# Performance work log

Hardware: AMD Instinct MI355X
Metric: run time of the kernel (lower is better)

## Reference

```python
import jax, jax.numpy as jnp
import numpy as np

RF = 512      # receptive field (power of 2)
F = 128       # filter_size
UP = 200      # upsample_size
MGC = 60      # mgc_size
NB = 4        # num_blocks
NL = 9        # log2(RF) CondConv layers per WaveNet block
T = 4         # number of mgc frames
N = T * UP    # number of sliding windows (800)
SQ = 0.70710678118


def setup_inputs() -> dict:
    key = jax.random.key(0)
    ks = jax.random.split(key, 12)
    r = lambda k, shp, s: jax.random.normal(k, shp, jnp.float32) * s
    return {
        "mgc": r(ks[0], (T, MGC), 1.0),
        "signal": r(ks[1], (N + RF,), 0.5),
        "cond_w": r(ks[2], (MGC * UP, MGC), 0.1),
        "cond_b": jnp.zeros((MGC * UP,), jnp.float32),
        "conv0_w": r(ks[3], (NB, 3, F, 1, 2), 0.3),
        "conv0_b": jnp.zeros((NB, 3, F), jnp.float32),
        "convL_w": r(ks[4], (NB, NL - 1, 3, F, F, 2), 0.08),
        "convL_b": jnp.zeros((NB, NL - 1, 3, F), jnp.float32),
        "condlin_w": r(ks[5], (NB, NL, 2, F, MGC), 0.1),
        "condlin_b": jnp.zeros((NB, NL, 2, F), jnp.float32),
        "pre_w": r(ks[6], (NB, 256, F), 0.08),
        "pre_b": jnp.zeros((NB, 256), jnp.float32),
        "mean_w": r(ks[7], (NB, 1, 256), 0.05),
        "mean_b": jnp.zeros((NB, 1), jnp.float32),
        "std_w": r(ks[8], (NB, 1, 256), 0.05),
        "std_b": jnp.zeros((NB, 1), jnp.float32),
        "eps": r(ks[9], (NB, N, 1), 1.0),
    }


def _cond_conv(h, W, b, cw, cb, cond):
    # h: [N, Cin, L]; W: [3, F, Cin, 2] (input/gate/residual stacked); b: [3, F]
    # kernel=2, stride=2 -> non-overlapping pairs; express as einsum GEMM
    n, c, L = h.shape
    hr = h.reshape(n, c, L // 2, 2)
    o = jnp.einsum('nclk,tock->tnol', hr, W) + b[:, None, :, None]  # [3, N, F, L/2]
    ci = cond @ cw[0].T + cb[0]  # [N, F]
    cg = cond @ cw[1].T + cb[1]  # [N, F]
    it = jnp.tanh(o[0] + ci[:, :, None])
    gt = jax.nn.sigmoid(o[1] + cg[:, :, None])
    return (it * gt + o[2]) * SQ


def _forward(mgc, signal, cond_w, cond_b, conv0_w, conv0_b, convL_w, convL_b,
             condlin_w, condlin_b, pre_w, pre_b, mean_w, mean_b, std_w, std_b, eps):
    # conditioning: Linear(60 -> 60*200) + tanh, reshaped to [T*200, 60]
    cond = jnp.tanh(mgc @ cond_w.T + cond_b).reshape(N, MGC)
    idx = jnp.arange(N)[:, None] + jnp.arange(RF)[None, :]  # sliding windows
    prev = signal
    tails = []
    mean = logvar = None
    for blk in range(NB):
        h = prev[idx][:, None, :]  # [N, 1, RF]
        for l in range(NL):
            W = conv0_w[blk] if l == 0 else convL_w[blk, l - 1]
            bb = conv0_b[blk] if l == 0 else convL_b[blk, l - 1]
            h = _cond_conv(h, W, bb, condlin_w[blk, l], condlin_b[blk, l], cond)
        pre = jax.nn.relu(h[:, :, 0] @ pre_w[blk].T + pre_b[blk])  # [N, 256]
        mean = pre @ mean_w[blk].T + mean_b[blk]    # [N, 1]
        logvar = pre @ std_w[blk].T + std_b[blk]    # [N, 1]
        new_x = eps[blk] * jnp.exp(0.5 * logvar) + mean  # reparameterize
        tails.append(jax.lax.stop_gradient(new_x[-RF:]))  # detached tail
        prev = jnp.concatenate([signal[:RF], new_x[:, 0]])
    return signal[RF:], mean, logvar, jnp.stack(tails)


def reference(mgc, signal, cond_w, cond_b, conv0_w, conv0_b, convL_w, convL_b,
              condlin_w, condlin_b, pre_w, pre_b, mean_w, mean_b, std_w, std_b, eps):
    return _forward(mgc, signal, cond_w, cond_b, conv0_w, conv0_b, convL_w, convL_b,
                    condlin_w, condlin_b, pre_w, pre_b, mean_w, mean_b, std_w, std_b, eps)
```

## Files before the change

kernel.cpp:

```cpp
#include <hip/hip_runtime.h>
#include <hip/hip_bf16.h>

#define F 128
#define MGCS 60
#define NWIN 800
#define RFS 512
#define NBLK 4
#define NLAY 9
#define SQF 0.70710678118f

typedef __attribute__((ext_vector_type(8))) short s16x8;
typedef __attribute__((ext_vector_type(4))) float f32x4;

#define VMCNT(n) asm volatile("s_waitcnt vmcnt(" #n ")" ::: "memory")

__device__ __forceinline__ float gated_act(float o0, float o1, float o2) {
  o0 = fminf(fmaxf(o0, -21.f), 21.f);
  o1 = fminf(fmaxf(o1, -21.f), 21.f);
  float a = __expf(2.f * o0);
  float b = __expf(-o1);
  float r = (a - 1.f) * __builtin_amdgcn_rcpf((a + 1.f) * (1.f + b));
  return (r + o2) * SQF;
}


__global__ void k_cond(const float* __restrict__ mgc, const float* __restrict__ cond_w,
                       const float* __restrict__ cond_b, float* __restrict__ cond) {
  int i = blockIdx.x * blockDim.x + threadIdx.x;
  if (i >= NWIN * MGCS) return;
  int n = i / MGCS, m = i % MGCS;
  int t = n / 200, u = n % 200;
  const float* wrow = cond_w + (size_t)(u * MGCS + m) * MGCS;
  const float* mr = mgc + t * MGCS;
  float s = cond_b[u * MGCS + m];
#pragma unroll
  for (int k = 0; k < MGCS; ++k) s += mr[k] * wrow[k];
  cond[i] = tanhf(s);
}

__global__ __launch_bounds__(256) void k_ci(
    const float* __restrict__ cond, const float* __restrict__ clw,
    const float* __restrict__ clb, float* __restrict__ CI) {
  int w = blockIdx.x;
  int n0 = blockIdx.y * 128;
  __shared__ float wsh[128][61];
  __shared__ float csh[128][61];
  int tid = threadIdx.x;
  for (int idx = tid; idx < 128 * MGCS; idx += 256) {
    int f = idx / MGCS, k = idx % MGCS;
    wsh[f][k] = clw[((size_t)w * 128 + f) * MGCS + k];
  }
  for (int idx = tid; idx < 128 * MGCS; idx += 256) {
    int n = idx / MGCS, k = idx % MGCS;
    csh[n][k] = (n0 + n < NWIN) ? cond[(n0 + n) * MGCS + k] : 0.f;
  }
  __syncthreads();
  int tn = tid >> 4, tf = tid & 15;
  float acc[8][8] = {};
  for (int k = 0; k < MGCS; ++k) {
    float a[8], b[8];
#pragma unroll
    for (int i = 0; i < 8; ++i) a[i] = csh[i * 16 + tn][k];
#pragma unroll
    for (int j = 0; j < 8; ++j) b[j] = wsh[j * 16 + tf][k];
#pragma unroll
    for (int i = 0; i < 8; ++i)
#pragma unroll
      for (int j = 0; j < 8; ++j) acc[i][j] += a[i] * b[j];
  }
  float bb[8];
#pragma unroll
  for (int j = 0; j < 8; ++j) bb[j] = clb[w * 128 + j * 16 + tf];
#pragma unroll
  for (int i = 0; i < 8; ++i) {
    int n = n0 + i * 16 + tn;
    if (n < NWIN) {
#pragma unroll
      for (int j = 0; j < 8; ++j)
        CI[((size_t)w * NWIN + n) * 128 + j * 16 + tf] = acc[i][j] + bb[j];
    }
  }
}

__global__ void k_wt(const float* __restrict__ convL_w, __hip_bfloat16* __restrict__ W2) {
  int i = blockIdx.x * blockDim.x + threadIdx.x;
  const int total = NBLK * 8 * 384 * 256;
  if (i >= total) return;
  int k = i & 255;
  int tf = (i >> 8) % 384;
  int wl = i / (384 * 256);
  int t = tf >> 7, f = tf & 127;
  int k2 = k >> 7, c = k & 127;
  W2[i] = __float2bfloat16(convL_w[(((size_t)(wl * 3 + t) * 128 + f) * 128 + c) * 2 + k2]);
}

__global__ void k_wt2(const float* __restrict__ pre_w, __hip_bfloat16* __restrict__ PW) {
  int i = blockIdx.x * blockDim.x + threadIdx.x;
  if (i < NBLK * 256 * 128) PW[i] = __float2bfloat16(pre_w[i]);
}

__global__ void k_outsig(const float* __restrict__ signal, float* __restrict__ out) {
  int i = blockIdx.x * blockDim.x + threadIdx.x;
  if (i < NWIN) out[i] = signal[RFS + i];
}


__global__ void k_pre0(const float* __restrict__ prev, const float* __restrict__ w0,
                       const float* __restrict__ b0, float* __restrict__ CV) {
  int i = blockIdx.x * blockDim.x + threadIdx.x;
  if (i >= 1310 * 384) return;
  int tf = i % 384, s = i / 384;
  CV[i] = b0[tf] + prev[s] * w0[tf * 2] + prev[s + 1] * w0[tf * 2 + 1];
}

__global__ void k_layer0(const float* __restrict__ CV, const float* __restrict__ CIb,
                         __hip_bfloat16* __restrict__ out) {
  int i = blockIdx.x * blockDim.x + threadIdx.x;
  if (i >= NWIN * 256 * 16) return;
  int fg = i & 15;
  int rest = i >> 4;
  int j = rest & 255;
  int n = rest >> 8;
  int f0 = fg * 8;
  const float* cv = CV + (size_t)(n + 2 * j) * 384;
  const float* ci = CIb + (size_t)n * F;
  float4 c0a = *(const float4*)(cv + f0),       c0b = *(const float4*)(cv + f0 + 4);
  float4 c1a = *(const float4*)(cv + 128 + f0), c1b = *(const float4*)(cv + 132 + f0);
  float4 c2a = *(const float4*)(cv + 256 + f0), c2b = *(const float4*)(cv + 260 + f0);
  float4 i0a = *(const float4*)(ci + f0),       i0b = *(const float4*)(ci + f0 + 4);
  float4 i1a = *(const float4*)(ci + (size_t)NWIN * F + f0);
  float4 i1b = *(const float4*)(ci + (size_t)NWIN * F + f0 + 4);
  s16x8 res;
#pragma unroll
  for (int e = 0; e < 8; ++e) {
    float o0 = ((e < 4) ? (&c0a.x)[e] : (&c0b.x)[e - 4]) + ((e < 4) ? (&i0a.x)[e] : (&i0b.x)[e - 4]);
    float o1 = ((e < 4) ? (&c1a.x)[e] : (&c1b.x)[e - 4]) + ((e < 4) ? (&i1a.x)[e] : (&i1b.x)[e - 4]);
    float o2 = (e < 4) ? (&c2a.x)[e] : (&c2b.x)[e - 4];
    __hip_bfloat16 h = __float2bfloat16(gated_act(o0, o1, o2));
    res[e] = *(short*)&h;
  }
  *(s16x8*)(out + ((size_t)(n * 256 + j)) * F + f0) = res;
}

template <int MFR, bool FLAT>
__device__ __forceinline__ void fuse_layer_b(
    const char* src, char* dst, const s16x8 (&breg)[3][8],
    const float* __restrict__ bb, const float* __restrict__ ciA,
    const float* __restrict__ ciB, int n, int mbase, int fbase, int lane) {
  const int col = lane & 15, kg = lane >> 4;
  const int f = fbase + col;
  const float b0 = bb[f], b1 = bb[128 + f], b2 = bb[256 + f];
  const float cA = ciA[n * 128 + f], cB = ciB[n * 128 + f];
  f32x4 acc[MFR][3];
#pragma unroll
  for (int mf = 0; mf < MFR; ++mf)
#pragma unroll
    for (int g = 0; g < 3; ++g) acc[mf][g] = (f32x4)(0.f);
#pragma unroll
  for (int ks = 0; ks < 8; ++ks) {
    s16x8 afr[MFR];
#pragma unroll
    for (int mf = 0; mf < MFR; ++mf) {
      int row = mbase + mf * 16 + col;
      afr[mf] = *(const s16x8*)(src + row * 512 + ((ks * 64 + kg * 16) ^ ((row & 7) << 4)));
    }
#pragma unroll
    for (int g = 0; g < 3; ++g)
#pragma unroll
      for (int mf = 0; mf < MFR; ++mf)
        acc[mf][g] = __builtin_amdgcn_mfma_f32_16x16x32_bf16(afr[mf], breg[g][ks], acc[mf][g], 0, 0, 0);
  }
#pragma unroll
  for (int mf = 0; mf < MFR; ++mf) {
#pragma unroll
    for (int r = 0; r < 4; ++r) {
      int orow = mbase + mf * 16 + kg * 4 + r;
      float o0 = acc[mf][0][r] + b0 + cA;
      float o1 = acc[mf][1][r] + b1 + cB;
      float o2 = acc[mf][2][r] + b2;
      __hip_bfloat16 h = __float2bfloat16(gated_act(o0, o1, o2));
      if (FLAT) {
        *(short*)(dst + orow * 256 + ((f * 2) ^ ((orow & 7) << 4))) = *(short*)&h;
      } else {
        int trow = orow >> 1;
        int kb = ((orow & 1) * 128 + f) * 2;
        *(short*)(dst + trow * 512 + (kb ^ ((trow & 7) << 4))) = *(short*)&h;
      }
    }
  }
}

#define CIL(l, t) (CIb + (size_t)((l) * 2 + (t)) * NWIN * F)

__global__ __launch_bounds__(512, 1) void k_fuse12(
    const __hip_bfloat16* __restrict__ A0, const __hip_bfloat16* __restrict__ W2b,
    const float* __restrict__ cb, const float* __restrict__ CIb,
    __hip_bfloat16* __restrict__ outC) {
  __shared__ char Ain[128 * 512];
  __shared__ char Bp[64 * 512];
  const int n = blockIdx.x;
  const int tid = threadIdx.x;
  const int lane = tid & 63, wid = tid >> 6;
  const int col = lane & 15, kg = lane >> 4;
  const int fbase = wid * 16;

  const char* srcg = (const char*)A0 + (size_t)n * 65536;
  const int half = lane >> 5, lin = (lane & 31) * 16;
#pragma unroll
  for (int it = 0; it < 8; ++it) {
    int inst = wid * 8 + it;
    int row = inst * 2 + half;
    __builtin_amdgcn_global_load_lds(
        (const __attribute__((address_space(1))) unsigned int*)(srcg + row * 512 + (lin ^ ((row & 7) << 4))),
        (__attribute__((address_space(3))) unsigned int*)(Ain + inst * 1024), 16, 0, 0);
  }

  s16x8 breg[3][8];
  {
    const char* W1 = (const char*)W2b;
#pragma unroll
    for (int g = 0; g < 3; ++g)
#pragma unroll
      for (int ks = 0; ks < 8; ++ks)
        breg[g][ks] = *(const s16x8*)(W1 + (size_t)(g * 128 + fbase + col) * 512 + ks * 64 + kg * 16);
  }
  VMCNT(0);
  __syncthreads();

  fuse_layer_b<4, false>(Ain, Bp, breg, cb, CIL(1, 0), CIL(1, 1), n, 0, fbase, lane);
  fuse_layer_b<4, false>(Ain, Bp, breg, cb, CIL(1, 0), CIL(1, 1), n, 64, fbase, lane);
  __syncthreads();

  {
    const char* W2l = (const char*)W2b + (size_t)384 * 512;
#pragma unroll
    for (int g = 0; g < 3; ++g)
#pragma unroll
      for (int ks = 0; ks < 8; ++ks)
        breg[g][ks] = *(const s16x8*)(W2l + (size_t)(g * 128 + fbase + col) * 512 + ks * 64 + kg * 16);
  }
  fuse_layer_b<4, true>(Bp, Ain, breg, cb + 384, CIL(2, 0), CIL(2, 1), n, 0, fbase, lane);
  __syncthreads();

#pragma unroll
  for (int p = 0; p < 2; ++p) {
    int idx = p * 512 + tid;
    int row = idx >> 4;
    int off = (idx & 15) * 16;
    s16x8 v = *(const s16x8*)(Ain + row * 256 + (off ^ ((row & 7) << 4)));
    *(s16x8*)((char*)outC + (size_t)n * 16384 + row * 256 + off) = v;
  }
}

template <int MFR, int FF, bool FLAT>
__device__ __forceinline__ void fuse_layer(
    const char* src, char* dst, const char* Wb, const float* __restrict__ bb,
    const float* __restrict__ ciA, const float* __restrict__ ciB,
    int n0, int logLW, int MV, int mbase, int fbase, int lane) {
  const int col = lane & 15, kg = lane >> 4;
  f32x4 acc[MFR][FF][3];
#pragma unroll
  for (int mf = 0; mf < MFR; ++mf)
#pragma unroll
    for (int ff = 0; ff < FF; ++ff)
#pragma unroll
      for (int g = 0; g < 3; ++g) acc[mf][ff][g] = (f32x4)(0.f);
#pragma unroll
  for (int ks = 0; ks < 8; ++ks) {
    s16x8 breg[FF][3];
#pragma unroll
    for (int ff = 0; ff < FF; ++ff)
#pragma unroll
      for (int g = 0; g < 3; ++g) {
        int tf = g * 128 + fbase + ff * 16 + col;
        breg[ff][g] = *(const s16x8*)(Wb + (size_t)tf * 512 + ks * 64 + kg * 16);
      }
    s16x8 afr[MFR];
#pragma unroll
    for (int mf = 0; mf < MFR; ++mf) {
      int row = mbase + mf * 16 + col;
      row = row < MV ? row : MV - 1;
      afr[mf] = *(const s16x8*)(src + row * 512 + ((ks * 64 + kg * 16) ^ ((row & 7) << 4)));
    }
#pragma unroll
    for (int ff = 0; ff < FF; ++ff)
#pragma unroll
      for (int g = 0; g < 3; ++g)
#pragma unroll
        for (int mf = 0; mf < MFR; ++mf)
          acc[mf][ff][g] = __builtin_amdgcn_mfma_f32_16x16x32_bf16(afr[mf], breg[ff][g], acc[mf][ff][g], 0, 0, 0);
  }
#pragma unroll
  for (int mf = 0; mf < MFR; ++mf)
#pragma unroll
    for (int ff = 0; ff < FF; ++ff) {
      int f = fbase + ff * 16 + col;
      float b0 = bb[f], b1 = bb[128 + f], b2 = bb[256 + f];
#pragma unroll
      for (int r = 0; r < 4; ++r) {
        int orow = mbase + mf * 16 + kg * 4 + r;
        if (orow < MV) {
          int n = n0 + (orow >> logLW);
          float o0 = acc[mf][ff][0][r] + b0 + ciA[n * 128 + f];
          float o1 = acc[mf][ff][1][r] + b1 + ciB[n * 128 + f];
          float o2 = acc[mf][ff][2][r] + b2;
          __hip_bfloat16 h = __float2bfloat16(gated_act(o0, o1, o2));
          if (FLAT) {
            *(short*)(dst + orow * 256 + ((f * 2) ^ ((orow & 7) << 4))) = *(short*)&h;
          } else {
            int trow = ((orow >> logLW) << (logLW - 1)) | ((orow & ((1 << logLW) - 1)) >> 1);
            int kb = ((orow & 1) * 128 + f) * 2;
            *(short*)(dst + trow * 512 + (kb ^ ((trow & 7) << 4))) = *(short*)&h;
          }
        }
      }
    }
}

__global__ __launch_bounds__(256, 3) void k_tail6(
    const __hip_bfloat16* __restrict__ C2, const __hip_bfloat16* __restrict__ W2b,
    const float* __restrict__ cb, const float* __restrict__ CIb,
    const __hip_bfloat16* __restrict__ PWb, const float* __restrict__ pb_,
    const float* __restrict__ mw_, const float* __restrict__ mb_,
    const float* __restrict__ sw_, const float* __restrict__ sb_,
    const float* __restrict__ eps_, const float* __restrict__ signal,
    float* __restrict__ prev_next, float* __restrict__ out_mean,
    float* __restrict__ out_logvar, float* __restrict__ out_tails) {
  __shared__ char Ain[64 * 512];
  __shared__ char Bp[32 * 512];
  __shared__ float psm[2][256];
  __shared__ float psv[2][256];
  const int b = blockIdx.x, n0 = b * 2;
  const int tid = threadIdx.x;
  const int lane = tid & 63, wid = tid >> 6;
  const int col = lane & 15, kg = lane >> 4;
  const char* srcg = (const char*)C2 + (size_t)n0 * 16384;
  const int half = lane >> 5, lin = (lane & 31) * 16;
#pragma unroll
  for (int it = 0; it < 8; ++it) {
    int inst = wid * 8 + it;
    int row = inst * 2 + half;
    __builtin_amdgcn_global_load_lds(
        (const __attribute__((address_space(1))) unsigned int*)(srcg + row * 512 + (lin ^ ((row & 7) << 4))),
        (__attribute__((address_space(3))) unsigned int*)(Ain + inst * 1024), 16, 0, 0);
  }
  VMCNT(0);
  __syncthreads();
  const int fbase = wid * 32;
#define WLp(lm) ((const char*)W2b + (size_t)(lm) * 384 * 512)
  fuse_layer<4, 2, false>(Ain, Bp, WLp(2), cb + 2 * 384, CIL(3, 0), CIL(3, 1), n0, 5, 64, 0, fbase, lane);
  __syncthreads();
  fuse_layer<2, 2, false>(Bp, Ain, WLp(3), cb + 3 * 384, CIL(4, 0), CIL(4, 1), n0, 4, 32, 0, fbase, lane);
  __syncthreads();
  fuse_layer<1, 2, false>(Ain, Bp, WLp(4), cb + 4 * 384, CIL(5, 0), CIL(5, 1), n0, 3, 16, 0, fbase, lane);
  __syncthreads();
  fuse_layer<1, 2, false>(Bp, Ain, WLp(5), cb + 5 * 384, CIL(6, 0), CIL(6, 1), n0, 2, 8, 0, fbase, lane);
  __syncthreads();
  fuse_layer<1, 2, false>(Ain, Bp, WLp(6), cb + 6 * 384, CIL(7, 0), CIL(7, 1), n0, 1, 4, 0, fbase, lane);
  __syncthreads();
  fuse_layer<1, 2, true>(Bp, Ain, WLp(7), cb + 7 * 384, CIL(8, 0), CIL(8, 1), n0, 0, 2, 0, fbase, lane);
  __syncthreads();

  {
    f32x4 acc2[4];
#pragma unroll
    for (int nf = 0; nf < 4; ++nf) acc2[nf] = (f32x4)(0.f);
    const char* PB = (const char*)PWb;
    int row = col < 2 ? col : 1;
#pragma unroll
    for (int ks = 0; ks < 4; ++ks) {
      s16x8 afr = *(const s16x8*)(Ain + row * 256 + ((ks * 64 + kg * 16) ^ ((row & 7) << 4)));
#pragma unroll
      for (int nf = 0; nf < 4; ++nf) {
        int o = wid * 64 + nf * 16 + col;
        s16x8 bfr = *(const s16x8*)(PB + (size_t)o * 256 + ks * 64 + kg * 16);
        acc2[nf] = __builtin_amdgcn_mfma_f32_16x16x32_bf16(afr, bfr, acc2[nf], 0, 0, 0);
      }
    }
#pragma unroll
    for (int nf = 0; nf < 4; ++nf) {
      int o = wid * 64 + nf * 16 + col;
      float pb = pb_[o], mw = mw_[o], sw = sw_[o];
#pragma unroll
      for (int r = 0; r < 4; ++r) {
        int m = kg * 4 + r;
        if (m < 2) {
          float p = fmaxf(acc2[nf][r] + pb, 0.f);
          psm[m][o] = p * mw;
          psv[m][o] = p * sw;
        }
      }
    }
  }
  __syncthreads();
  if (wid < 2) {
    float sm = 0.f, sv = 0.f;
#pragma unroll
    for (int e = 0; e < 4; ++e) {
      sm += psm[wid][lane * 4 + e];
      sv += psv[wid][lane * 4 + e];
    }
#pragma unroll
    for (int off = 32; off > 0; off >>= 1) {
      sm += __shfl_down(sm, off);
      sv += __shfl_down(sv, off);
    }
    if (lane == 0) {
      int nn = n0 + wid;
      float mean = sm + mb_[0];
      float logv = sv + sb_[0];
      float nx = eps_[nn] * expf(0.5f * logv) + mean;
      if (prev_next) prev_next[RFS + nn] = nx;
      if (out_mean) { out_mean[nn] = mean; out_logvar[nn] = logv; }
      if (nn >= NWIN - RFS) out_tails[nn - (NWIN - RFS)] = nx;
    }
  }
  if (prev_next && tid < 2 && n0 + tid < RFS)
    prev_next[n0 + tid] = signal[n0 + tid];
}


extern "C" void kernel_launch(void* const* d_in, const int* in_sizes, int n_in,
                              void* d_out, int out_size, void* d_ws, size_t ws_size,
                              hipStream_t stream) {
  const float* mgc      = (const float*)d_in[0];
  const float* signal   = (const float*)d_in[1];
  const float* cond_w   = (const float*)d_in[2];
  const float* cond_b   = (const float*)d_in[3];
  const float* conv0_w  = (const float*)d_in[4];
  const float* conv0_b  = (const float*)d_in[5];
  const float* convL_w  = (const float*)d_in[6];
  const float* convL_b  = (const float*)d_in[7];
  const float* condlin_w= (const float*)d_in[8];
  const float* condlin_b= (const float*)d_in[9];
  const float* pre_w    = (const float*)d_in[10];
  const float* pre_b    = (const float*)d_in[11];
  const float* mean_w   = (const float*)d_in[12];
  const float* mean_b   = (const float*)d_in[13];
  const float* std_w    = (const float*)d_in[14];
  const float* std_b    = (const float*)d_in[15];
  const float* eps      = (const float*)d_in[16];
  float* out = (float*)d_out;

  float* wsf   = (float*)d_ws;
  float* cond  = wsf;
  float* CI    = cond + 48000;
  float* prevb = CI + 7372800;
  float* CV    = prevb + 5248;
  float* base  = CV + 503040;
  __hip_bfloat16* W2   = (__hip_bfloat16*)base;
  __hip_bfloat16* PW   = W2 + 3145728;
  __hip_bfloat16* bufA = PW + 131072;
  __hip_bfloat16* bufC = bufA + 26214400 + 65536;

  k_cond<<<(NWIN * MGCS + 255) / 256, 256, 0, stream>>>(mgc, cond_w, cond_b, cond);
  k_ci<<<dim3(72, 7), 256, 0, stream>>>(cond, condlin_w, condlin_b, CI);
  k_wt<<<(NBLK * 8 * 384 * 256 + 255) / 256, 256, 0, stream>>>(convL_w, W2);
  k_wt2<<<(NBLK * 256 * 128 + 255) / 256, 256, 0, stream>>>(pre_w, PW);
  k_outsig<<<(NWIN + 255) / 256, 256, 0, stream>>>(signal, out);

  for (int blk = 0; blk < NBLK; ++blk) {
    const float* prev = (blk == 0) ? signal : (prevb + (size_t)(blk - 1) * 1312);
    const float* CIb = CI + (size_t)(blk * NLAY) * 2 * NWIN * F;
    k_pre0<<<(1310 * 384 + 255) / 256, 256, 0, stream>>>(
        prev, conv0_w + (size_t)blk * 3 * F * 2, conv0_b + (size_t)blk * 3 * F, CV);
    k_layer0<<<(NWIN * 256 * 16 + 255) / 256, 256, 0, stream>>>(CV, CIb, bufA);

    k_fuse12<<<NWIN, 512, 0, stream>>>(
        bufA, W2 + (size_t)blk * 8 * 384 * 256, convL_b + (size_t)blk * 8 * 384, CIb, bufC);

    k_tail6<<<NWIN / 2, 256, 0, stream>>>(
        bufC, W2 + (size_t)blk * 8 * 384 * 256,
        convL_b + (size_t)blk * 8 * 384, CIb,
        PW + (size_t)blk * 256 * 128, pre_b + (size_t)blk * 256,
        mean_w + (size_t)blk * 256, mean_b + blk,
        std_w + (size_t)blk * 256, std_b + blk,
        eps + (size_t)blk * NWIN, signal,
        (blk < 3) ? (prevb + (size_t)blk * 1312) : nullptr,
        (blk == 3) ? (out + 800) : nullptr,
        (blk == 3) ? (out + 1600) : nullptr,
        out + 2400 + (size_t)blk * 512);
  }
}
```

Before: 760.9 us.

## Fuse layer0 gating into per-window mega kernel and extend it through layer four

Removes the separate layer0 kernel. Each window's block now computes the first gated activation directly from a bf16 CV buffer into LDS, instead of materialising a large bf16 intermediate (tens of MB) in global memory. The per-window kernel now runs conv layers one through four in LDS, prefetching each layer's weight registers before the barrier. The tail kernel handles the remaining layers and processes four windows per block. This cuts global round-trips and launches, at the cost of bf16 rounding of the layer0 pre-activation and more serial work per block.

New measurement: 810.0 us. 1.06x slower.

```diff
diff --git a/kernel.cpp b/kernel.cpp
--- a/kernel.cpp
+++ b/kernel.cpp
@@ -21,6 +21,12 @@
   float b = __expf(-o1);
   float r = (a - 1.f) * __builtin_amdgcn_rcpf((a + 1.f) * (1.f + b));
   return (r + o2) * SQF;
+}
+
+__device__ __forceinline__ float bf2f(short s) {
+  union { unsigned u; float f; } t;
+  t.u = ((unsigned)(unsigned short)s) << 16;
+  return t.f;
 }
 
 
@@ -106,40 +112,11 @@
 
 
 __global__ void k_pre0(const float* __restrict__ prev, const float* __restrict__ w0,
-                       const float* __restrict__ b0, float* __restrict__ CV) {
+                       const float* __restrict__ b0, __hip_bfloat16* __restrict__ CVh) {
   int i = blockIdx.x * blockDim.x + threadIdx.x;
   if (i >= 1310 * 384) return;
   int tf = i % 384, s = i / 384;
-  CV[i] = b0[tf] + prev[s] * w0[tf * 2] + prev[s + 1] * w0[tf * 2 + 1];
-}
-
-__global__ void k_layer0(const float* __restrict__ CV, const float* __restrict__ CIb,
-                         __hip_bfloat16* __restrict__ out) {
-  int i = blockIdx.x * blockDim.x + threadIdx.x;
-  if (i >= NWIN * 256 * 16) return;
-  int fg = i & 15;
-  int rest = i >> 4;
-  int j = rest & 255;
-  int n = rest >> 8;
-  int f0 = fg * 8;
-  const float* cv = CV + (size_t)(n + 2 * j) * 384;
-  const float* ci = CIb + (size_t)n * F;
-  float4 c0a = *(const float4*)(cv + f0),       c0b = *(const float4*)(cv + f0 + 4);
-  float4 c1a = *(const float4*)(cv + 128 + f0), c1b = *(const float4*)(cv + 132 + f0);
-  float4 c2a = *(const float4*)(cv + 256 + f0), c2b = *(const float4*)(cv + 260 + f0);
-  float4 i0a = *(const float4*)(ci + f0),       i0b = *(const float4*)(ci + f0 + 4);
-  float4 i1a = *(const float4*)(ci + (size_t)NWIN * F + f0);
-  float4 i1b = *(const float4*)(ci + (size_t)NWIN * F + f0 + 4);
-  s16x8 res;
-#pragma unroll
-  for (int e = 0; e < 8; ++e) {
-    float o0 = ((e < 4) ? (&c0a.x)[e] : (&c0b.x)[e - 4]) + ((e < 4) ? (&i0a.x)[e] : (&i0b.x)[e - 4]);
-    float o1 = ((e < 4) ? (&c1a.x)[e] : (&c1b.x)[e - 4]) + ((e < 4) ? (&i1a.x)[e] : (&i1b.x)[e - 4]);
-    float o2 = (e < 4) ? (&c2a.x)[e] : (&c2b.x)[e - 4];
-    __hip_bfloat16 h = __float2bfloat16(gated_act(o0, o1, o2));
-    res[e] = *(short*)&h;
-  }
-  *(s16x8*)(out + ((size_t)(n * 256 + j)) * F + f0) = res;
+  CVh[i] = __float2bfloat16(b0[tf] + prev[s] * w0[tf * 2] + prev[s + 1] * w0[tf * 2 + 1]);
 }
 
 template <int MFR, bool FLAT>
@@ -192,10 +169,19 @@
 
 #define CIL(l, t) (CIb + (size_t)((l) * 2 + (t)) * NWIN * F)
 
-__global__ __launch_bounds__(512, 1) void k_fuse12(
-    const __hip_bfloat16* __restrict__ A0, const __hip_bfloat16* __restrict__ W2b,
+#define LOADB(lm)                                                                   \
+  {                                                                                 \
+    const char* Wl = (const char*)W2b + (size_t)(lm) * 384 * 512;                   \
+    _Pragma("unroll") for (int g = 0; g < 3; ++g)                                   \
+        _Pragma("unroll") for (int ks = 0; ks < 8; ++ks)                            \
+            breg[g][ks] = *(const s16x8*)(Wl + (size_t)(g * 128 + fbase + col) * 512 \
+                                          + ks * 64 + kg * 16);                     \
+  }
+
+__global__ __launch_bounds__(512, 1) void k_mega(
+    const __hip_bfloat16* __restrict__ CVh, const __hip_bfloat16* __restrict__ W2b,
     const float* __restrict__ cb, const float* __restrict__ CIb,
-    __hip_bfloat16* __restrict__ outC) {
+    char* __restrict__ bufD) {
   __shared__ char Ain[128 * 512];
   __shared__ char Bp[64 * 512];
   const int n = blockIdx.x;
@@ -203,53 +189,53 @@
   const int lane = tid & 63, wid = tid >> 6;
   const int col = lane & 15, kg = lane >> 4;
   const int fbase = wid * 16;
-
-  const char* srcg = (const char*)A0 + (size_t)n * 65536;
-  const int half = lane >> 5, lin = (lane & 31) * 16;
-#pragma unroll
-  for (int it = 0; it < 8; ++it) {
-    int inst = wid * 8 + it;
-    int row = inst * 2 + half;
-    __builtin_amdgcn_global_load_lds(
-        (const __attribute__((address_space(1))) unsigned int*)(srcg + row * 512 + (lin ^ ((row & 7) << 4))),
-        (__attribute__((address_space(3))) unsigned int*)(Ain + inst * 1024), 16, 0, 0);
-  }
-
   s16x8 breg[3][8];
+  LOADB(0);
+
   {
-    const char* W1 = (const char*)W2b;
-#pragma unroll
-    for (int g = 0; g < 3; ++g)
-#pragma unroll
-      for (int ks = 0; ks < 8; ++ks)
-        breg[g][ks] = *(const s16x8*)(W1 + (size_t)(g * 128 + fbase + col) * 512 + ks * 64 + kg * 16);
-  }
-  VMCNT(0);
+    const int j = tid >> 1;
+    const int fh = (tid & 1) * 64;
+    const __hip_bfloat16* cvr = CVh + (size_t)(n + 2 * j) * 384;
+    const float* ci0 = CIL(0, 0) + n * 128;
+    const float* ci1 = CIL(0, 1) + n * 128;
+    const int row = j >> 1;
+    const int kb0 = (j & 1) * 128;
+#pragma unroll
+    for (int e8 = 0; e8 < 8; ++e8) {
+      int f = fh + e8 * 8;
+      s16x8 c0 = *(const s16x8*)(cvr + f);
+      s16x8 c1 = *(const s16x8*)(cvr + 128 + f);
+      s16x8 c2 = *(const s16x8*)(cvr + 256 + f);
+      float4 i0a = *(const float4*)(ci0 + f), i0b = *(const float4*)(ci0 + f + 4);
+      float4 i1a = *(const float4*)(ci1 + f), i1b = *(const float4*)(ci1 + f + 4);
+      s16x8 res;
+#pragma unroll
+      for (int e = 0; e < 8; ++e) {
+        float o0 = bf2f(c0[e]) + ((e < 4) ? (&i0a.x)[e] : (&i0b.x)[e - 4]);
+        float o1 = bf2f(c1[e]) + ((e < 4) ? (&i1a.x)[e] : (&i1b.x)[e - 4]);
+        float o2 = bf2f(c2[e]);
+        __hip_bfloat16 h = __float2bfloat16(gated_act(o0, o1, o2));
+        res[e] = *(short*)&h;
+      }
+      *(s16x8*)(Ain + row * 512 + (((kb0 + f) * 2) ^ ((row & 7) << 4))) = res;
+    }
+  }
   __syncthreads();
 
   fuse_layer_b<4, false>(Ain, Bp, breg, cb, CIL(1, 0), CIL(1, 1), n, 0, fbase, lane);
   fuse_layer_b<4, false>(Ain, Bp, breg, cb, CIL(1, 0), CIL(1, 1), n, 64, fbase, lane);
-  __syncthreads();
-
-  {
-    const char* W2l = (const char*)W2b + (size_t)384 * 512;
-#pragma unroll
-    for (int g = 0; g < 3; ++g)
-#pragma unroll
-      for (int ks = 0; ks < 8; ++ks)
-        breg[g][ks] = *(const s16x8*)(W2l + (size_t)(g * 128 + fbase + col) * 512 + ks * 64 + kg * 16);
-  }
-  fuse_layer_b<4, true>(Bp, Ain, breg, cb + 384, CIL(2, 0), CIL(2, 1), n, 0, fbase, lane);
-  __syncthreads();
-
-#pragma unroll
-  for (int p = 0; p < 2; ++p) {
-    int idx = p * 512 + tid;
-    int row = idx >> 4;
-    int off = (idx & 15) * 16;
-    s16x8 v = *(const s16x8*)(Ain + row * 256 + (off ^ ((row & 7) << 4)));
-    *(s16x8*)((char*)outC + (size_t)n * 16384 + row * 256 + off) = v;
-  }
+  LOADB(1);
+  __syncthreads();
+  fuse_layer_b<4, false>(Bp, Ain, breg, cb + 384, CIL(2, 0), CIL(2, 1), n, 0, fbase, lane);
+  LOADB(2);
+  __syncthreads();
+  fuse_layer_b<2, false>(Ain, Bp, breg, cb + 2 * 384, CIL(3, 0), CIL(3, 1), n, 0, fbase, lane);
+  LOADB(3);
+  __syncthreads();
+  fuse_layer_b<1, false>(Bp, Ain, breg, cb + 3 * 384, CIL(4, 0), CIL(4, 1), n, 0, fbase, lane);
+  __syncthreads();
+  if (tid < 256)
+    *(s16x8*)(bufD + (size_t)n * 4096 + tid * 16) = *(const s16x8*)(Ain + tid * 16);
 }
 
 template <int MFR, int FF, bool FLAT>
@@ -317,8 +303,8 @@
     }
 }
 
-__global__ __launch_bounds__(256, 3) void k_tail6(
-    const __hip_bfloat16* __restrict__ C2, const __hip_bfloat16* __restrict__ W2b,
+__global__ __launch_bounds__(256, 3) void k_tail5(
+    const char* __restrict__ D, const __hip_bfloat16* __restrict__ W2b,
     const float* __restrict__ cb, const float* __restrict__ CIb,
     const __hip_bfloat16* __restrict__ PWb, const float* __restrict__ pb_,
     const float* __restrict__ mw_, const float* __restrict__ mb_,
@@ -326,39 +312,33 @@
     const float* __restrict__ eps_, const float* __restrict__ signal,
     float* __restrict__ prev_next, float* __restrict__ out_mean,
     float* __restrict__ out_logvar, float* __restrict__ out_tails) {
-  __shared__ char Ain[64 * 512];
-  __shared__ char Bp[32 * 512];
-  __shared__ float psm[2][256];
-  __shared__ float psv[2][256];
-  const int b = blockIdx.x, n0 = b * 2;
+  __shared__ char Ain[32 * 512];
+  __shared__ char Bp[16 * 512];
+  __shared__ float psm[4][256];
+  __shared__ float psv[4][256];
+  const int b = blockIdx.x, n0 = b * 4;
   const int tid = threadIdx.x;
   const int lane = tid & 63, wid = tid >> 6;
   const int col = lane & 15, kg = lane >> 4;
-  const char* srcg = (const char*)C2 + (size_t)n0 * 16384;
-  const int half = lane >> 5, lin = (lane & 31) * 16;
-#pragma unroll
-  for (int it = 0; it < 8; ++it) {
-    int inst = wid * 8 + it;
-    int row = inst * 2 + half;
+  const char* srcg = D + (size_t)n0 * 4096;
+#pragma unroll
+  for (int it = 0; it < 4; ++it) {
+    int inst = wid * 4 + it;
     __builtin_amdgcn_global_load_lds(
-        (const __attribute__((address_space(1))) unsigned int*)(srcg + row * 512 + (lin ^ ((row & 7) << 4))),
+        (const __attribute__((address_space(1))) unsigned int*)(srcg + inst * 1024 + lane * 16),
         (__attribute__((address_space(3))) unsigned int*)(Ain + inst * 1024), 16, 0, 0);
   }
   VMCNT(0);
   __syncthreads();
   const int fbase = wid * 32;
 #define WLp(lm) ((const char*)W2b + (size_t)(lm) * 384 * 512)
-  fuse_layer<4, 2, false>(Ain, Bp, WLp(2), cb + 2 * 384, CIL(3, 0), CIL(3, 1), n0, 5, 64, 0, fbase, lane);
-  __syncthreads();
-  fuse_layer<2, 2, false>(Bp, Ain, WLp(3), cb + 3 * 384, CIL(4, 0), CIL(4, 1), n0, 4, 32, 0, fbase, lane);
-  __syncthreads();
-  fuse_layer<1, 2, false>(Ain, Bp, WLp(4), cb + 4 * 384, CIL(5, 0), CIL(5, 1), n0, 3, 16, 0, fbase, lane);
-  __syncthreads();
-  fuse_layer<1, 2, false>(Bp, Ain, WLp(5), cb + 5 * 384, CIL(6, 0), CIL(6, 1), n0, 2, 8, 0, fbase, lane);
-  __syncthreads();
-  fuse_layer<1, 2, false>(Ain, Bp, WLp(6), cb + 6 * 384, CIL(7, 0), CIL(7, 1), n0, 1, 4, 0, fbase, lane);
-  __syncthreads();
-  fuse_layer<1, 2, true>(Bp, Ain, WLp(7), cb + 7 * 384, CIL(8, 0), CIL(8, 1), n0, 0, 2, 0, fbase, lane);
+  fuse_layer<2, 2, false>(Ain, Bp, WLp(4), cb + 4 * 384, CIL(5, 0), CIL(5, 1), n0, 3, 32, 0, fbase, lane);
+  __syncthreads();
+  fuse_layer<1, 2, false>(Bp, Ain, WLp(5), cb + 5 * 384, CIL(6, 0), CIL(6, 1), n0, 2, 16, 0, fbase, lane);
+  __syncthreads();
+  fuse_layer<1, 2, false>(Ain, Bp, WLp(6), cb + 6 * 384, CIL(7, 0), CIL(7, 1), n0, 1, 8, 0, fbase, lane);
+  __syncthreads();
+  fuse_layer<1, 2, true>(Bp, Ain, WLp(7), cb + 7 * 384, CIL(8, 0), CIL(8, 1), n0, 0, 4, 0, fbase, lane);
   __syncthreads();
 
   {
@@ -366,7 +346,7 @@
 #pragma unroll
     for (int nf = 0; nf < 4; ++nf) acc2[nf] = (f32x4)(0.f);
     const char* PB = (const char*)PWb;
-    int row = col < 2 ? col : 1;
+    int row = col < 4 ? col : 3;
 #pragma unroll
     for (int ks = 0; ks < 4; ++ks) {
       s16x8 afr = *(const s16x8*)(Ain + row * 256 + ((ks * 64 + kg * 16) ^ ((row & 7) << 4)));
@@ -384,7 +364,7 @@
 #pragma unroll
       for (int r = 0; r < 4; ++r) {
         int m = kg * 4 + r;
-        if (m < 2) {
+        if (m < 4) {
           float p = fmaxf(acc2[nf][r] + pb, 0.f);
           psm[m][o] = p * mw;
           psv[m][o] = p * sw;
@@ -393,7 +373,7 @@
     }
   }
   __syncthreads();
-  if (wid < 2) {
+  {
     float sm = 0.f, sv = 0.f;
 #pragma unroll
     for (int e = 0; e < 4; ++e) {
@@ -415,7 +395,7 @@
       if (nn >= NWIN - RFS) out_tails[nn - (NWIN - RFS)] = nx;
     }
   }
-  if (prev_next && tid < 2 && n0 + tid < RFS)
+  if (prev_next && tid < 4 && n0 + tid < RFS)
     prev_next[n0 + tid] = signal[n0 + tid];
 }
 
@@ -446,12 +426,10 @@
   float* cond  = wsf;
   float* CI    = cond + 48000;
   float* prevb = CI + 7372800;
-  float* CV    = prevb + 5248;
-  float* base  = CV + 503040;
-  __hip_bfloat16* W2   = (__hip_bfloat16*)base;
-  __hip_bfloat16* PW   = W2 + 3145728;
-  __hip_bfloat16* bufA = PW + 131072;
-  __hip_bfloat16* bufC = bufA + 26214400 + 65536;
+  __hip_bfloat16* W2  = (__hip_bfloat16*)(prevb + 5248);
+  __hip_bfloat16* PW  = W2 + 3145728;
+  __hip_bfloat16* CVh = PW + 131072;
+  char* bufD = (char*)(CVh + 503040);
 
   k_cond<<<(NWIN * MGCS + 255) / 256, 256, 0, stream>>>(mgc, cond_w, cond_b, cond);
   k_ci<<<dim3(72, 7), 256, 0, stream>>>(cond, condlin_w, condlin_b, CI);
@@ -463,14 +441,13 @@
     const float* prev = (blk == 0) ? signal : (prevb + (size_t)(blk - 1) * 1312);
     const float* CIb = CI + (size_t)(blk * NLAY) * 2 * NWIN * F;
     k_pre0<<<(1310 * 384 + 255) / 256, 256, 0, stream>>>(
-        prev, conv0_w + (size_t)blk * 3 * F * 2, conv0_b + (size_t)blk * 3 * F, CV);
-    k_layer0<<<(NWIN * 256 * 16 + 255) / 256, 256, 0, stream>>>(CV, CIb, bufA);
-
-    k_fuse12<<<NWIN, 512, 0, stream>>>(
-        bufA, W2 + (size_t)blk * 8 * 384 * 256, convL_b + (size_t)blk * 8 * 384, CIb, bufC);
-
-    k_tail6<<<NWIN / 2, 256, 0, stream>>>(
-        bufC, W2 + (size_t)blk * 8 * 384 * 256,
+        prev, conv0_w + (size_t)blk * 3 * F * 2, conv0_b + (size_t)blk * 3 * F, CVh);
+
+    k_mega<<<NWIN, 512, 0, stream>>>(
+        CVh, W2 + (size_t)blk * 8 * 384 * 256, convL_b + (size_t)blk * 8 * 384, CIb, bufD);
+
+    k_tail5<<<NWIN / 4, 256, 0, stream>>>(
+        bufD, W2 + (size_t)blk * 8 * 384 * 256,
         convL_b + (size_t)blk * 8 * 384, CIb,
         PW + (size_t)blk * 256 * 128, pre_b + (size_t)blk * 256,
         mean_w + (size_t)blk * 256, mean_b + blk,
```
